# Kernel optimization log

Measured on AMD Instinct MI355X. Metric: run time of the kernel, lower is better.

The kernel has to match this reference:

```python
import jax, jax.numpy as jnp
import numpy as np

B, N, C, H = 16, 1024, 768, 12
HD = C // H               # head_dim = 64
SCALE = HD ** -0.5
EPS = 1e-5


def ter_quant(w):
    """BitNet-b1.58 ternary weight quantization with straight-through estimator.
    Per-tensor scale = mean(|W|); weights rounded to {-1,0,1}*scale."""
    s = jnp.mean(jnp.abs(w))
    wq = jnp.round(jnp.clip(w / (s + EPS), -1.0, 1.0)) * s
    return w + jax.lax.stop_gradient(wq - w)


def setup_inputs() -> dict:
    key = jax.random.key(0)
    k1, k2, k3 = jax.random.split(key, 3)
    return {
        "x": jax.random.normal(k1, (B, N, C), dtype=jnp.float32),
        "w_qkv": jax.random.normal(k2, (3 * C, C), dtype=jnp.float32) * 0.02,
        "w_proj": jax.random.normal(k3, (C, C), dtype=jnp.float32) * 0.02,
        "b_proj": jnp.zeros((C,), dtype=jnp.float32),
    }


def reference(x, w_qkv, w_proj, b_proj):
    # ternary-quantized QKV projection: [B,N,C] @ [C,3C] -> [B,N,3C]
    qkv = jnp.einsum('bnc,dc->bnd', x, ter_quant(w_qkv))
    qkv = qkv.reshape(B, N, 3, H, HD).transpose(2, 0, 3, 1, 4)  # [3,B,H,N,HD]
    q, k, v = qkv[0], qkv[1], qkv[2]
    # manual softmax attention (dropout p=0 -> identity)
    attn = jax.nn.softmax(jnp.einsum('bhqd,bhkd->bhqk', q, k) * SCALE, axis=-1)
    out = jnp.einsum('bhqk,bhkd->bhqd', attn, v)          # [B,H,N,HD]
    out = out.transpose(0, 2, 1, 3).reshape(B, N, C)      # [B,N,C]
    # ternary-quantized output projection
    return jnp.einsum('bnc,dc->bnd', out, ter_quant(w_proj)) + b_proj
```

## Files before the change

### kernel.cpp

```cpp
#include <hip/hip_runtime.h>
#include <hip/hip_bf16.h>

#define DEVI __device__ __forceinline__

typedef __bf16 bf16_t;
typedef __bf16 bf16x8 __attribute__((ext_vector_type(8)));
typedef float  f32x4  __attribute__((ext_vector_type(4)));
typedef float  f32x16 __attribute__((ext_vector_type(16)));
typedef unsigned short u16x4 __attribute__((ext_vector_type(4)));
typedef unsigned int   u32x4 __attribute__((ext_vector_type(4)));

typedef __attribute__((address_space(1))) unsigned int gas_u32;
typedef __attribute__((address_space(3))) unsigned int las_u32;

#define LOG2E 1.4426950408889634f

DEVI void gload16(const void* g, void* l) {
  __builtin_amdgcn_global_load_lds((gas_u32*)g, (las_u32*)l, 16, 0, 0);
}

DEVI unsigned short bf16bits(float f) {
  bf16_t b = (bf16_t)f;
  return __builtin_bit_cast(unsigned short, b);
}

DEVI unsigned pk2(float a, float b) {
  return ((unsigned)bf16bits(b) << 16) | (unsigned)bf16bits(a);
}

DEVI unsigned short quant1(float wv, double s) {
  double tq = (double)wv / s;
  tq = fmin(fmax(tq, -1.0), 1.0);
  return __builtin_bit_cast(unsigned short, (bf16_t)(float)rint(tq));
}

__global__ __launch_bounds__(256) void k_abssum2(const float* __restrict__ wq,
                                                 const float* __restrict__ wp,
                                                 double* __restrict__ partials) {
  __shared__ double sm[256];
  const int t = threadIdx.x, bid = blockIdx.x;
  const float* __restrict__ w = (bid < 256) ? wq : wp;
  const int n = (bid < 256) ? 1769472 : 589824;
  const int b0 = bid & 255;
  double acc = 0.0;
  for (int i = b0 * 256 + t; i < n; i += 65536)
    acc += (double)fabsf(w[i]);
  sm[t] = acc;
  __syncthreads();
  #pragma unroll
  for (int s = 128; s > 0; s >>= 1) {
    if (t < s) sm[t] += sm[t + s];
    __syncthreads();
  }
  if (t == 0) partials[bid] = sm[0];
}

__global__ __launch_bounds__(256) void k_reduce2(const double* __restrict__ partials,
                                                 double* __restrict__ outs) {
  __shared__ double sm[256];
  const int t = threadIdx.x;
  sm[t] = partials[blockIdx.x * 256 + t];
  __syncthreads();
  #pragma unroll
  for (int s = 128; s > 0; s >>= 1) {
    if (t < s) sm[t] += sm[t + s];
    __syncthreads();
  }
  if (t == 0) outs[blockIdx.x] = sm[0];
}

__global__ __launch_bounds__(256) void k_prep(
    const float* __restrict__ wq, const float* __restrict__ wp,
    const float* __restrict__ x, const double* __restrict__ scl,
    bf16_t* __restrict__ wqs, bf16_t* __restrict__ wps, bf16_t* __restrict__ xbf) {
  const int bid = blockIdx.x, t = threadIdx.x;
  if (bid < 1728) {
    const double s = scl[0] * (1.0 / 1769472.0) + 1e-5;
    const int i = bid * 256 + t;
    const float4 v = ((const float4*)wq)[i];
    u16x4 o = { quant1(v.x, s), quant1(v.y, s), quant1(v.z, s), quant1(v.w, s) };
    ((u16x4*)wqs)[i] = o;
  } else if (bid < 2304) {
    const double s = scl[1] * (1.0 / 589824.0) + 1e-5;
    const int i = (bid - 1728) * 256 + t;
    const float4 v = ((const float4*)wp)[i];
    u16x4 o = { quant1(v.x, s), quant1(v.y, s), quant1(v.z, s), quant1(v.w, s) };
    ((u16x4*)wps)[i] = o;
  } else {
    const int i = (bid - 2304) * 256 + t;
    const float4 v = ((const float4*)x)[i];
    u16x4 pk = { bf16bits(v.x), bf16bits(v.y), bf16bits(v.z), bf16bits(v.w) };
    ((u16x4*)xbf)[i] = pk;
  }
}

template<int MODE>
__global__ __launch_bounds__(512, 4) void k_gemm(
    const bf16_t* __restrict__ A, const bf16_t* __restrict__ Bw,
    const double* __restrict__ sumptr, double invn,
    bf16_t* __restrict__ Qb, bf16_t* __restrict__ Kb, bf16_t* __restrict__ VTb,
    const float* __restrict__ bias, float* __restrict__ Out,
    int nxblk)
{
  __shared__ __align__(16) char lds[73728];
  const int t = threadIdx.x, l = t & 63, w = t >> 6;

  const int nblk = nxblk * 64;
  const int flat = blockIdx.y * nxblk + blockIdx.x;
  const int per = nblk >> 3;
  const int swz = (flat & 7) * per + (flat >> 3);
  const int m0 = (swz / nxblk) * 256, n0 = (swz % nxblk) * 128;

  const int wm = w >> 1, wn = w & 1;
  const int lq = l & 15, lh = l >> 4;
  const int grow = t >> 2, gs8 = (t & 3) * 8;

  auto stage = [&](int slot, int kts) {
    char* dst = lds + slot * 24576;
    gload16(A + (size_t)(m0 + grow) * 768 + kts * 32 + gs8, dst + t * 16);
    gload16(A + (size_t)(m0 + 128 + grow) * 768 + kts * 32 + gs8, dst + 8192 + t * 16);
    gload16(Bw + (size_t)(n0 + grow) * 768 + kts * 32 + gs8, dst + 16384 + t * 16);
  };

  f32x4 acc[4][4] = {};

  stage(0, 0);
  stage(1, 1);
  asm volatile("s_waitcnt vmcnt(3)" ::: "memory");
  asm volatile("s_barrier" ::: "memory");

  #pragma unroll
  for (int kt = 0; kt < 24; ++kt) {
    const char* cA = lds + (kt % 3) * 24576 + (wm >> 1) * 8192;
    const char* cB = lds + (kt % 3) * 24576 + 16384;

    bf16x8 af[4], bf[4];
    #pragma unroll
    for (int i = 0; i < 4; ++i) {
      const int lrow = (wm & 1) * 64 + i * 16 + lq;
      af[i] = *(const bf16x8*)(cA + lrow * 64 + lh * 16);
    }
    #pragma unroll
    for (int j = 0; j < 4; ++j) {
      const int row = wn * 64 + j * 16 + lq;
      bf[j] = *(const bf16x8*)(cB + row * 64 + lh * 16);
    }
    if (kt < 22) stage((kt + 2) % 3, kt + 2);
    __builtin_amdgcn_s_setprio(1);
    #pragma unroll
    for (int i = 0; i < 4; ++i)
      #pragma unroll
      for (int j = 0; j < 4; ++j)
        acc[i][j] = __builtin_amdgcn_mfma_f32_16x16x32_bf16(af[i], bf[j], acc[i][j], 0, 0, 0);
    __builtin_amdgcn_s_setprio(0);
    if (kt <= 21)      asm volatile("s_waitcnt vmcnt(3)" ::: "memory");
    else if (kt == 22) asm volatile("s_waitcnt vmcnt(0)" ::: "memory");
    asm volatile("s_barrier" ::: "memory");
  }

  const float s = (float)((*sumptr) * invn);
  char* st = lds + w * 8192;

  const int mrow0 = m0 + wm * 64;
  const int b = mrow0 >> 10, nbase = mrow0 & 1023;

  if (MODE == 0) {
    const int d0 = n0 + wn * 64;
    const int which = d0 / 768;
    const int hh = (d0 >> 6) % 12;
    if (which == 2) {
      #pragma unroll
      for (int j = 0; j < 4; ++j)
        #pragma unroll
        for (int i = 0; i < 4; ++i)
          #pragma unroll
          for (int r = 0; r < 4; ++r) {
            const int rowd = j * 16 + lq;
            const int coln = (i * 16 + lh * 4 + r) * 2;
            *(bf16_t*)(st + rowd * 128 + (coln ^ ((rowd & 7) << 4))) =
                (bf16_t)(acc[i][j][r] * s);
          }
    } else {
      const float sc = (which == 0) ? s * 0.125f * LOG2E : s;
      #pragma unroll
      for (int i = 0; i < 4; ++i)
        #pragma unroll
        for (int j = 0; j < 4; ++j)
          #pragma unroll
          for (int r = 0; r < 4; ++r) {
            const int row = i * 16 + lh * 4 + r;
            const int colb = (j * 16 + lq) * 2;
            *(bf16_t*)(st + row * 128 + (colb ^ ((row & 7) << 4))) =
                (bf16_t)(acc[i][j][r] * sc);
          }
    }
    __syncthreads();
    if (which == 0) {
      char* dstp = (char*)(Qb + ((size_t)(b * 12 + hh) * 1024 + nbase) * 64);
      #pragma unroll
      for (int it = 0; it < 8; ++it) {
        const int row = it * 8 + (l >> 3);
        const int colb = (l & 7) * 16;
        const u32x4 v = *(const u32x4*)(st + row * 128 + (colb ^ ((row & 7) << 4)));
        *(u32x4*)(dstp + row * 128 + colb) = v;
      }
    } else {
      bf16_t* base = (which == 1) ? Kb : VTb;
      char* dstp = (char*)base + ((((size_t)(b * 12 + hh)) * 16 + (nbase >> 6)) << 13);
      #pragma unroll
      for (int j = 0; j < 8; ++j) {
        const int row = (j >> 2) * 32 + (l & 31);
        const int colb = (j & 3) * 32 + (l >> 5) * 16;
        const u32x4 v = *(const u32x4*)(st + row * 128 + (colb ^ ((row & 7) << 4)));
        *(u32x4*)(dstp + j * 1024 + l * 16) = v;
      }
    }
  } else {
    const int d0 = n0 + wn * 64;
    const float4 bv = *(const float4*)(bias + d0 + (l & 15) * 4);
    #pragma unroll
    for (int c = 0; c < 2; ++c) {
      #pragma unroll
      for (int i2 = 0; i2 < 2; ++i2) {
        const int i = c * 2 + i2;
        #pragma unroll
        for (int j = 0; j < 4; ++j)
          #pragma unroll
          for (int r = 0; r < 4; ++r) {
            const int row = i2 * 16 + lh * 4 + r;
            const int colb = (j * 16 + lq) * 4;
            *(float*)(st + row * 256 + (colb ^ ((row & 7) << 4))) = acc[i][j][r] * s;
          }
      }
      __syncthreads();
      #pragma unroll
      for (int it = 0; it < 8; ++it) {
        const int row = it * 4 + (l >> 4);
        const int colb = (l & 15) * 16;
        float4 v = *(const float4*)(st + row * 256 + (colb ^ ((row & 7) << 4)));
        v.x += bv.x; v.y += bv.y; v.z += bv.z; v.w += bv.w;
        *(float4*)((char*)(Out + (size_t)(mrow0 + c * 32 + row) * 768 + d0) + colb) = v;
      }
      __syncthreads();
    }
  }
}

__global__ __launch_bounds__(256, 4) void k_attn(
    const bf16_t* __restrict__ Qb, const bf16_t* __restrict__ Kb,
    const bf16_t* __restrict__ VTb, bf16_t* __restrict__ Ob)
{
  __shared__ bf16_t smem[2][2][4096];
  const int t = threadIdx.x, l = t & 63, w = t >> 6;
  const int bh = blockIdx.x, qb = blockIdx.y;
  const int lq = l & 31, hi = l >> 5;
  const int q0 = qb * 128 + w * 32;

  const char* Kg = (const char*)(Kb + (size_t)bh * 65536);
  const char* Vg = (const char*)(VTb + (size_t)bh * 65536);

  bf16x8 qf[4];
  #pragma unroll
  for (int ks = 0; ks < 4; ++ks)
    qf[ks] = *(const bf16x8*)(Qb + (size_t)bh * 65536 + (q0 + lq) * 64 + ks * 16 + hi * 8);

  f32x16 ot0 = {}, ot1 = {};
  float lrun = 0.0f;

  auto stage = [&](int buf, int kt) {
    #pragma unroll
    for (int i = 0; i < 2; ++i) {
      const int c = i * 4 + w;
      gload16(Kg + (size_t)kt * 8192 + c * 1024 + l * 16, &smem[buf][0][c * 512]);
      gload16(Vg + (size_t)kt * 8192 + c * 1024 + l * 16, &smem[buf][1][c * 512]);
    }
  };

  stage(0, 0);
  __syncthreads();

  for (int kt = 0; kt < 16; ++kt) {
    const int cur = kt & 1;
    if (kt < 15) stage(cur ^ 1, kt + 1);
    const char* lK = (const char*)smem[cur][0];
    const char* lV = (const char*)smem[cur][1];
    const int lo = l * 16;

    f32x16 st0 = {}, st1 = {};
    __builtin_amdgcn_s_setprio(1);
    #pragma unroll
    for (int ks = 0; ks < 4; ++ks) {
      const bf16x8 k0 = *(const bf16x8*)(lK + ks * 1024 + lo);
      const bf16x8 k1 = *(const bf16x8*)(lK + (4 + ks) * 1024 + lo);
      st0 = __builtin_amdgcn_mfma_f32_32x32x16_bf16(k0, qf[ks], st0, 0, 0, 0);
      st1 = __builtin_amdgcn_mfma_f32_32x32x16_bf16(k1, qf[ks], st1, 0, 0, 0);
    }
    __builtin_amdgcn_s_setprio(0);

    float psum = 0.0f;
    __builtin_amdgcn_s_setprio(1);
    auto grp = [&](const f32x16& stv, int r0, int g) {
      float p[8];
      #pragma unroll
      for (int e = 0; e < 8; ++e) p[e] = __builtin_amdgcn_exp2f(stv[r0 + e]);
      psum += ((p[0] + p[1]) + (p[2] + p[3])) + ((p[4] + p[5]) + (p[6] + p[7]));
      const unsigned w0 = pk2(p[0], p[1]), w1 = pk2(p[2], p[3]);
      const unsigned w2 = pk2(p[4], p[5]), w3 = pk2(p[6], p[7]);
      const unsigned x0 = __shfl_xor(w0, 32), x1 = __shfl_xor(w1, 32);
      const unsigned x2 = __shfl_xor(w2, 32), x3 = __shfl_xor(w3, 32);
      const u32x4 fw = hi ? u32x4{x2, x3, w2, w3} : u32x4{w0, w1, x0, x1};
      const bf16x8 pf = __builtin_bit_cast(bf16x8, fw);
      const bf16x8 v0 = *(const bf16x8*)(lV + g * 1024 + lo);
      const bf16x8 v1 = *(const bf16x8*)(lV + (4 + g) * 1024 + lo);
      ot0 = __builtin_amdgcn_mfma_f32_32x32x16_bf16(v0, pf, ot0, 0, 0, 0);
      ot1 = __builtin_amdgcn_mfma_f32_32x32x16_bf16(v1, pf, ot1, 0, 0, 0);
    };
    grp(st0, 0, 0);
    grp(st0, 8, 1);
    grp(st1, 0, 2);
    grp(st1, 8, 3);
    __builtin_amdgcn_s_setprio(0);
    psum += __shfl_xor(psum, 32);
    lrun += psum;

    __syncthreads();
  }

  __syncthreads();
  bf16_t* olds = (bf16_t*)smem + w * 2048;
  const float inv = 1.0f / lrun;
  #pragma unroll
  for (int dt = 0; dt < 2; ++dt)
    #pragma unroll
    for (int rg = 0; rg < 4; ++rg) {
      u16x4 pk;
      #pragma unroll
      for (int e = 0; e < 4; ++e)
        pk[e] = bf16bits((dt ? ot1[rg * 4 + e] : ot0[rg * 4 + e]) * inv);
      const int d = rg * 8 + hi * 4 + dt * 32;
      *(u16x4*)((char*)olds + ((lq * 128 + d * 2) ^ ((lq & 7) << 4))) = pk;
    }
  __syncthreads();
  const int b = bh / 12, h = bh % 12;
  #pragma unroll
  for (int i = 0; i < 8; ++i) {
    const int q = i * 4 + (l >> 4);
    const u16x4 v =
        *(const u16x4*)((const char*)olds + ((q * 128 + (l & 15) * 8) ^ ((q & 7) << 4)));
    *(u16x4*)(Ob + ((size_t)(b * 1024 + q0 + q)) * 768 + h * 64 + (l & 15) * 4) = v;
  }
}

extern "C" void kernel_launch(void* const* d_in, const int* in_sizes, int n_in,
                              void* d_out, int out_size, void* d_ws, size_t ws_size,
                              hipStream_t stream) {
  const float* x      = (const float*)d_in[0];
  const float* w_qkv  = (const float*)d_in[1];
  const float* w_proj = (const float*)d_in[2];
  const float* b_proj = (const float*)d_in[3];
  float* out = (float*)d_out;

  char* ws = (char*)d_ws;
  double* part  = (double*)ws;
  double* scl   = (double*)(ws + 4096);
  bf16_t* xbf   = (bf16_t*)(ws + 4608);
  bf16_t* wqs   = (bf16_t*)(ws + 4608 + 25165824);
  bf16_t* wps   = (bf16_t*)(ws + 4608 + 25165824 + 3538944);
  bf16_t* qbuf  = (bf16_t*)(ws + 4608 + 25165824 + 3538944 + 1179648);
  bf16_t* kbuf  = qbuf + 12582912;
  bf16_t* vtbuf = kbuf + 12582912;
  bf16_t* aout  = xbf;

  k_abssum2<<<512, 256, 0, stream>>>(w_qkv, w_proj, part);
  k_reduce2<<<2, 256, 0, stream>>>(part, scl);
  k_prep<<<14592, 256, 0, stream>>>(w_qkv, w_proj, x, scl, wqs, wps, xbf);
  k_gemm<0><<<dim3(18, 64), 512, 0, stream>>>(xbf, wqs, scl, 1.0 / 1769472.0,
                                              qbuf, kbuf, vtbuf, nullptr, nullptr, 18);
  k_attn<<<dim3(192, 8), 256, 0, stream>>>(qbuf, kbuf, vtbuf, aout);
  k_gemm<1><<<dim3(6, 64), 512, 0, stream>>>(aout, wps, scl + 1, 1.0 / 589824.0,
                                             nullptr, nullptr, nullptr, b_proj, out, 6);
}
```

Baseline: 188.4 us.

## Software-pipeline attention QK^T one tile ahead with triple-buffered K/V staging

Restructures the attention loop to compute the next tile's QK^T scores while doing softmax and PV for the current tile, using a three-slot LDS ring that prefetches two tiles ahead. This aims to overlap exp/shuffle work with MFMA and to hide global-load latency. It costs extra registers for a second score buffer and more LDS, so occupancy drops from 4 to 3 blocks. The abs-sum reduction kernel also switches to float4 vectorized loads.

```diff
diff --git a/kernel.cpp b/kernel.cpp
--- a/kernel.cpp
+++ b/kernel.cpp
@@ -39,12 +39,15 @@
                                                  double* __restrict__ partials) {
   __shared__ double sm[256];
   const int t = threadIdx.x, bid = blockIdx.x;
-  const float* __restrict__ w = (bid < 256) ? wq : wp;
-  const int n = (bid < 256) ? 1769472 : 589824;
+  const float4* __restrict__ w = (const float4*)((bid < 256) ? wq : wp);
+  const int n4 = (bid < 256) ? 442368 : 147456;
   const int b0 = bid & 255;
   double acc = 0.0;
-  for (int i = b0 * 256 + t; i < n; i += 65536)
-    acc += (double)fabsf(w[i]);
+  for (int i = b0 * 256 + t; i < n4; i += 65536) {
+    const float4 v = w[i];
+    acc += ((double)fabsf(v.x) + (double)fabsf(v.y)) +
+           ((double)fabsf(v.z) + (double)fabsf(v.w));
+  }
   sm[t] = acc;
   __syncthreads();
   #pragma unroll
@@ -246,11 +249,11 @@
   }
 }
 
-__global__ __launch_bounds__(256, 4) void k_attn(
+__global__ __launch_bounds__(256, 3) void k_attn(
     const bf16_t* __restrict__ Qb, const bf16_t* __restrict__ Kb,
     const bf16_t* __restrict__ VTb, bf16_t* __restrict__ Ob)
 {
-  __shared__ bf16_t smem[2][2][4096];
+  __shared__ bf16_t smem[3][2][4096];
   const int t = threadIdx.x, l = t & 63, w = t >> 6;
   const int bh = blockIdx.x, qb = blockIdx.y;
   const int lq = l & 31, hi = l >> 5;
@@ -266,39 +269,31 @@
 
   f32x16 ot0 = {}, ot1 = {};
   float lrun = 0.0f;
-
-  auto stage = [&](int buf, int kt) {
+  const int lo = l * 16;
+
+  auto stage = [&](int slot, int kt) {
     #pragma unroll
     for (int i = 0; i < 2; ++i) {
       const int c = i * 4 + w;
-      gload16(Kg + (size_t)kt * 8192 + c * 1024 + l * 16, &smem[buf][0][c * 512]);
-      gload16(Vg + (size_t)kt * 8192 + c * 1024 + l * 16, &smem[buf][1][c * 512]);
+      gload16(Kg + (size_t)kt * 8192 + c * 1024 + l * 16, &smem[slot][0][c * 512]);
+      gload16(Vg + (size_t)kt * 8192 + c * 1024 + l * 16, &smem[slot][1][c * 512]);
     }
   };
 
-  stage(0, 0);
-  __syncthreads();
-
-  for (int kt = 0; kt < 16; ++kt) {
-    const int cur = kt & 1;
-    if (kt < 15) stage(cur ^ 1, kt + 1);
-    const char* lK = (const char*)smem[cur][0];
-    const char* lV = (const char*)smem[cur][1];
-    const int lo = l * 16;
-
-    f32x16 st0 = {}, st1 = {};
-    __builtin_amdgcn_s_setprio(1);
+  auto qkt = [&](const bf16_t* bufK, f32x16& s0, f32x16& s1) {
+    const char* lK = (const char*)bufK;
     #pragma unroll
     for (int ks = 0; ks < 4; ++ks) {
       const bf16x8 k0 = *(const bf16x8*)(lK + ks * 1024 + lo);
       const bf16x8 k1 = *(const bf16x8*)(lK + (4 + ks) * 1024 + lo);
-      st0 = __builtin_amdgcn_mfma_f32_32x32x16_bf16(k0, qf[ks], st0, 0, 0, 0);
-      st1 = __builtin_amdgcn_mfma_f32_32x32x16_bf16(k1, qf[ks], st1, 0, 0, 0);
-    }
-    __builtin_amdgcn_s_setprio(0);
-
+      s0 = __builtin_amdgcn_mfma_f32_32x32x16_bf16(k0, qf[ks], s0, 0, 0, 0);
+      s1 = __builtin_amdgcn_mfma_f32_32x32x16_bf16(k1, qf[ks], s1, 0, 0, 0);
+    }
+  };
+
+  auto sfpv = [&](const f32x16& s0, const f32x16& s1, const bf16_t* bufV) {
+    const char* lV = (const char*)bufV;
     float psum = 0.0f;
-    __builtin_amdgcn_s_setprio(1);
     auto grp = [&](const f32x16& stv, int r0, int g) {
       float p[8];
       #pragma unroll
@@ -315,14 +310,35 @@
       ot0 = __builtin_amdgcn_mfma_f32_32x32x16_bf16(v0, pf, ot0, 0, 0, 0);
       ot1 = __builtin_amdgcn_mfma_f32_32x32x16_bf16(v1, pf, ot1, 0, 0, 0);
     };
-    grp(st0, 0, 0);
-    grp(st0, 8, 1);
-    grp(st1, 0, 2);
-    grp(st1, 8, 3);
-    __builtin_amdgcn_s_setprio(0);
+    grp(s0, 0, 0);
+    grp(s0, 8, 1);
+    grp(s1, 0, 2);
+    grp(s1, 8, 3);
     psum += __shfl_xor(psum, 32);
     lrun += psum;
-
+  };
+
+  stage(0, 0);
+  stage(1, 1);
+  __syncthreads();
+
+  f32x16 sbuf[2][2];
+  sbuf[0][0] = f32x16{};
+  sbuf[0][1] = f32x16{};
+  qkt(smem[0][0], sbuf[0][0], sbuf[0][1]);
+
+  #pragma unroll
+  for (int kt = 0; kt < 16; ++kt) {
+    const int cur = kt & 1, nxt = cur ^ 1;
+    if (kt + 2 < 16) stage((kt + 2) % 3, kt + 2);
+    if (kt + 1 < 16) {
+      sbuf[nxt][0] = f32x16{};
+      sbuf[nxt][1] = f32x16{};
+      __builtin_amdgcn_s_setprio(1);
+      qkt(smem[(kt + 1) % 3][0], sbuf[nxt][0], sbuf[nxt][1]);
+      __builtin_amdgcn_s_setprio(0);
+    }
+    sfpv(sbuf[cur][0], sbuf[cur][1], smem[kt % 3][1]);
     __syncthreads();
   }
 
```

Result: slower. 193.8 us (+2.8%).
